# Kernel optimization log

Hardware: AMD Instinct MI355X
Metric: run time of the kernel (lower is better)

## Reference

```python
import jax, jax.numpy as jnp
import numpy as np

N = 50000          # masked node count
E = 800000         # edges (avg degree 16)
IN_DIM, GCN_DIM, REL_DIM, TRAIN_DIM, OUT_DIM = 3, 128, 64, 128, 2
BATCHES = 1


def setup_inputs() -> dict:
    key = jax.random.key(0)
    ks = jax.random.split(key, 16)
    s = 0.05
    return {
        "features": jax.random.normal(ks[0], (N, IN_DIM), jnp.float32),
        "edge_index": jax.random.randint(ks[1], (2, E), 0, N, dtype=jnp.int32),
        "trainOT": jax.random.normal(ks[2], (TRAIN_DIM,), jnp.float32),
        "W1": jax.random.normal(ks[3], (IN_DIM, GCN_DIM), jnp.float32) * s,
        "b1": jnp.zeros((GCN_DIM,), jnp.float32),
        "W2": jax.random.normal(ks[4], (GCN_DIM, GCN_DIM), jnp.float32) * s,
        "b2": jnp.zeros((GCN_DIM,), jnp.float32),
        "Wq": jax.random.normal(ks[5], (GCN_DIM, REL_DIM), jnp.float32) * s,
        "bq": jnp.zeros((REL_DIM,), jnp.float32),
        "Wk": jax.random.normal(ks[6], (TRAIN_DIM, REL_DIM), jnp.float32) * s,
        "bk": jnp.zeros((REL_DIM,), jnp.float32),
        "Wv": jax.random.normal(ks[7], (GCN_DIM, TRAIN_DIM), jnp.float32) * s,
        "bv": jnp.zeros((TRAIN_DIM,), jnp.float32),
        "Ws": jax.random.normal(ks[8], (TRAIN_DIM, OUT_DIM * N), jnp.float32) * s,
        "bs": jnp.zeros((OUT_DIM * N,), jnp.float32),
    }


def _gcn_conv(x, W, b, src, dst, n):
    """PyG GCNConv: h = D^-1/2 (A+I) D^-1/2 (x W) + b (self-loops already in src/dst)."""
    h = x @ W                                                  # [n, d_out]
    ones = jnp.ones(src.shape[0], dtype=x.dtype)
    deg = jax.ops.segment_sum(ones, dst, num_segments=n)      # in-degree incl. self-loop
    dinv = jnp.where(deg > 0, jax.lax.rsqrt(deg), 0.0)
    norm = dinv[src] * dinv[dst]                               # [E+n]
    msg = h[src] * norm[:, None]                               # gather (dominant traffic)
    return jax.ops.segment_sum(msg, dst, num_segments=n) + b   # scatter-add


def reference(features, edge_index, trainOT, W1, b1, W2, b2, Wq, bq, Wk, bk, Wv, bv, Ws, bs):
    n = features.shape[0]
    loop = jnp.arange(n, dtype=edge_index.dtype)
    src = jnp.concatenate([edge_index[0], loop])
    dst = jnp.concatenate([edge_index[1], loop])

    h1 = jax.nn.relu(_gcn_conv(features, W1, b1, src, dst, n))   # gcn1 + relu
    h2 = _gcn_conv(h1, W2, b2, src, dst, n)                      # gcn2

    q = h2 @ Wq + bq                                             # [n, rel]
    v = h2 @ Wv + bv                                             # [n, train]
    k = trainOT @ Wk + bk                                        # [rel]
    scale = jnp.asarray(Wq.shape[1], q.dtype) ** 0.5
    rel = jax.nn.sigmoid((q @ k) / scale)                        # [n]
    summed_idea = (rel[:, None] * v).sum(axis=0)                 # [train]
    new_trainOT = trainOT + summed_idea
    speak = new_trainOT @ Ws + bs                                # [out_dim * num_nodes]
    out = speak.reshape(BATCHES, -1, OUT_DIM)
    return out, new_trainOT
```

## Files before the change

kernel.cpp:

```cpp
#include <hip/hip_runtime.h>
#include <math.h>

#define O_RPD    (0)
#define O_DINV   (512*1024)
#define O_SMALL  (768*1024)
#define O_Y      (1024*1024)
#define O_RELW   (1280*1024)
#define O_REL    (1536*1024)
#define O_GHD    (1792*1024)
#define O_GHS    (2048*1024)
#define O_GOD    (2304*1024)
#define O_GOS    (2560*1024)
#define O_BSD    (2816*1024)
#define O_BSS    (2944*1024)
#define O_PART   (3072*1024)
#define O_XS     (3712*1024)
#define O_G1     (4608*1024)
#define O_SRTD   (5632*1024)
#define O_SRTS   (9216*1024)
#define O_COLD   (12544*1024)

#define NCHUNK 256

static __device__ __forceinline__ int blockExclScan256(int v, volatile int* lds, int t) {
    int lane = t & 63, wid = t >> 6;
    int incl = v;
#pragma unroll
    for (int off = 1; off < 64; off <<= 1) {
        int n = __shfl_up(incl, off);
        if (lane >= off) incl += n;
    }
    if (lane == 63) lds[wid] = incl;
    __syncthreads();
    if (t == 0) {
        int s = 0;
#pragma unroll
        for (int i = 0; i < 4; ++i) { int x = lds[i]; lds[i] = s; s += x; }
    }
    __syncthreads();
    return lds[wid] + incl - v;
}

__global__ void k_hist(const int* __restrict__ eidx, int* __restrict__ ghD,
                       int* __restrict__ ghS,
                       const float* __restrict__ trainOT, const float* __restrict__ Wq,
                       const float* __restrict__ bq, const float* __restrict__ Wk,
                       const float* __restrict__ bk, const float* __restrict__ W2,
                       const float* __restrict__ b2, float* __restrict__ small,
                       int E, int CS, int NB) {
    int b = blockIdx.x, t = threadIdx.x;
    if (b == NCHUNK) {
        if (blockIdx.y) return;
        __shared__ float kv[64];
        __shared__ float wqk[128];
        __shared__ float fred[256];
        if (t < 64) {
            float acc = bk[t];
            for (int j = 0; j < 128; ++j) acc += trainOT[j] * Wk[j * 64 + t];
            kv[t] = acc;
        }
        __syncthreads();
        if (t < 128) {
            float aq = 0.f;
            for (int c2 = 0; c2 < 64; ++c2) aq += Wq[t * 64 + c2] * kv[c2];
            wqk[t] = aq;
        }
        fred[t] = (t < 64) ? bq[t] * kv[t] : 0.f;
        __syncthreads();
        for (int off = 128; off >= 1; off >>= 1) { if (t < off) fred[t] += fred[t + off]; __syncthreads(); }
        float bqs = fred[0];
        __syncthreads();
        if (t < 128) {
            float a2 = 0.f;
            for (int j = 0; j < 128; ++j) a2 += W2[t * 128 + j] * wqk[j];
            small[t] = a2;
        }
        fred[t] = (t < 128) ? b2[t] * wqk[t] : 0.f;
        __syncthreads();
        for (int off = 128; off >= 1; off >>= 1) { if (t < off) fred[t] += fred[t + off]; __syncthreads(); }
        if (t == 0) small[128] = bqs + fred[0];
        return;
    }
    __shared__ int lh[256];
    const int* arr = blockIdx.y ? eidx : (eidx + E);
    int* gh = blockIdx.y ? ghS : ghD;
    lh[t] = 0; __syncthreads();
    int s = b * CS, e = min(E, s + CS);
    for (int i = s + t; i < e; i += 256) atomicAdd(&lh[arr[i] >> 8], 1);
    __syncthreads();
    if (t < NB) gh[t * NCHUNK + b] = lh[t];
}

__global__ void k_goff(const int* __restrict__ ghD, const int* __restrict__ ghS,
                       int* __restrict__ goD, int* __restrict__ goS,
                       int* __restrict__ bsD, int* __restrict__ bsS, int E, int NB) {
    __shared__ int lred[256];
    __shared__ int lds1[4];
    int nb = blockIdx.x, t = threadIdx.x;
    const int* gh = blockIdx.y ? ghS : ghD;
    int* go = blockIdx.y ? goS : goD;
    int* bs = blockIdx.y ? bsS : bsD;
    int rs = 0;
    if (t < nb) {
        const int4* row = reinterpret_cast<const int4*>(gh + t * NCHUNK);
        for (int i = 0; i < NCHUNK / 4; ++i) { int4 p = row[i]; rs += p.x + p.y + p.z + p.w; }
    }
    lred[t] = rs; __syncthreads();
    for (int off = 128; off >= 1; off >>= 1) { if (t < off) lred[t] += lred[t + off]; __syncthreads(); }
    int base = lred[0];
    __syncthreads();
    if (t == 0) { bs[nb] = base; if (nb == NB - 1) bs[NB] = E; }
    int g = gh[nb * NCHUNK + t];
    int gx = blockExclScan256(g, lds1, t);
    go[nb * NCHUNK + t] = base + gx;
}

__global__ void k_scatter(const int* __restrict__ eidx, const int* __restrict__ goD,
                          const int* __restrict__ goS, unsigned int* __restrict__ srtD,
                          unsigned int* __restrict__ srtS, int E, int CS, int NB) {
    __shared__ int lcur[256];
    int b = blockIdx.x, t = threadIdx.x;
    const int* key = blockIdx.y ? eidx : (eidx + E);
    const int* val = blockIdx.y ? (eidx + E) : eidx;
    const int* go  = blockIdx.y ? goS : goD;
    unsigned int* srt = blockIdx.y ? srtS : srtD;
    if (t < NB) lcur[t] = go[t * NCHUNK + b];
    __syncthreads();
    int s = b * CS, e = min(E, s + CS);
    for (int i = s + t; i < e; i += 256) {
        int k = key[i];
        int pos = atomicAdd(&lcur[k >> 8], 1);
        srt[pos] = ((unsigned int)(k & 255) << 16) | (unsigned int)val[i];
    }
}

__global__ void k_build(const unsigned int* __restrict__ srtD, const int* __restrict__ bsD,
                        int* __restrict__ rpD, int* __restrict__ colD,
                        float* __restrict__ dinv, const float* __restrict__ x,
                        float4* __restrict__ xs4, int N) {
    __shared__ int lcnt[256];
    __shared__ int lpos[256];
    __shared__ int lds1[4];
    int nb = blockIdx.x, t = threadIdx.x;
    lcnt[t] = 0; __syncthreads();
    int s = bsD[nb], e = bsD[nb + 1];
    for (int i = s + t; i < e; i += 256) atomicAdd(&lcnt[srtD[i] >> 16], 1);
    __syncthreads();
    int c = lcnt[t];
    int cx = blockExclScan256(c, lds1, t);
    int rpv = s + cx;
    int node = (nb << 8) + t;
    rpD[node] = rpv;
    lpos[t] = rpv;
    if (node < N) {
        float d = rsqrtf((float)(c + 1));
        dinv[node] = d;
        float4 v;
        v.x = x[node * 3] * d; v.y = x[node * 3 + 1] * d; v.z = x[node * 3 + 2] * d; v.w = 0.f;
        xs4[node] = v;
    }
    __syncthreads();
    for (int i = s + t; i < e; i += 256) {
        unsigned int v = srtD[i];
        int p = atomicAdd(&lpos[v >> 16], 1);
        colD[p] = (int)(v & 0xffffu);
    }
}

__global__ void k_y(const float4* __restrict__ xs4, const int* __restrict__ rpD,
                    const int* __restrict__ colD, const float* __restrict__ dinv,
                    const float* __restrict__ W1, const float* __restrict__ b1,
                    const float* __restrict__ small, float4* __restrict__ g1,
                    float* __restrict__ y, int N) {
    int t = threadIdx.x;
    int sub = t & 15;
    int node = blockIdx.x * 16 + (t >> 4);
    if (node >= N) return;
    float di = dinv[node];
    int s = rpD[node], e = rpD[node + 1];
    float a0 = 0.f, a1 = 0.f, a2 = 0.f;
    for (int j = s + sub; j < e; j += 16) {
        float4 xv = xs4[colD[j]];
        a0 += xv.x; a1 += xv.y; a2 += xv.z;
    }
    if (sub == 0) { float4 xv = xs4[node]; a0 += xv.x; a1 += xv.y; a2 += xv.z; }
#pragma unroll
    for (int off = 1; off < 16; off <<= 1) {
        a0 += __shfl_xor(a0, off);
        a1 += __shfl_xor(a1, off);
        a2 += __shfl_xor(a2, off);
    }
    a0 *= di; a1 *= di; a2 *= di;
    float yl = 0.f;
#pragma unroll
    for (int m = 0; m < 8; ++m) {
        int c = sub * 8 + m;
        float h = fmaxf(a0 * W1[c] + a1 * W1[128 + c] + a2 * W1[256 + c] + b1[c], 0.f);
        yl += h * small[c];
    }
#pragma unroll
    for (int off = 1; off < 16; off <<= 1) yl += __shfl_xor(yl, off);
    if (sub == 0) {
        y[node] = yl * di;
        float4 gv; gv.x = a0; gv.y = a1; gv.z = a2; gv.w = di;
        g1[node] = gv;
    }
}

__global__ void k_dv(const float* __restrict__ y, const int* __restrict__ rpD,
                     const int* __restrict__ colD, const float* __restrict__ dinv,
                     const float* __restrict__ small, float* __restrict__ relw,
                     float* __restrict__ rel, int N) {
    int t = threadIdx.x;
    int sub = t & 15;
    int node = blockIdx.x * 16 + (t >> 4);
    if (node >= N) return;
    float di = dinv[node];
    int s = rpD[node], e = rpD[node + 1];
    float acc = (sub == 0) ? y[node] : 0.f;
    for (int j = s + sub; j < e; j += 16) acc += y[colD[j]];
#pragma unroll
    for (int off = 1; off < 16; off <<= 1) acc += __shfl_xor(acc, off);
    float z = (acc * di + small[128]) * 0.125f;
    float r = 1.f / (1.f + __expf(-z));
    if (sub == 0) { rel[node] = r; relw[node] = r * di; }
}

__global__ void k_zS(const unsigned int* __restrict__ srtS, const int* __restrict__ bsS,
                     const float* __restrict__ relw, const float* __restrict__ rel,
                     const float4* __restrict__ g1, const float* __restrict__ W1,
                     const float* __restrict__ b1, float* __restrict__ part, int N) {
    __shared__ float zl[256];
    __shared__ float W1s[384];
    __shared__ float b1s[128];
    __shared__ float sS[4][132];
    int nb = blockIdx.x, t = threadIdx.x, lane = t & 63, wid = t >> 6;
    int sub = lane & 15, gid = wid * 4 + (lane >> 4);
    int node0 = (nb << 8) + t;
    zl[t] = (node0 < N) ? relw[node0] : 0.f;
    if (t < 128) { W1s[t] = W1[t]; W1s[128 + t] = W1[128 + t]; W1s[256 + t] = W1[256 + t];
                   b1s[t] = b1[t]; }
    __syncthreads();
    int s = bsS[nb], e = bsS[nb + 1];
    for (int i = s + t; i < e; i += 256) {
        unsigned int v = srtS[i];
        atomicAdd(&zl[v >> 16], relw[v & 0xffffu]);
    }
    __syncthreads();
    float sacc[8];
#pragma unroll
    for (int m = 0; m < 8; ++m) sacc[m] = 0.f;
    float Racc = 0.f;
#pragma unroll 4
    for (int r = 0; r < 16; ++r) {
        int nl = gid * 16 + r;
        int node = (nb << 8) + nl;
        if (node < N) {
            float4 gv = g1[node];
            float zw = zl[nl] * gv.w;
#pragma unroll
            for (int m = 0; m < 8; ++m) {
                int c = sub * 8 + m;
                float h = fmaxf(gv.x * W1s[c] + gv.y * W1s[128 + c] + gv.z * W1s[256 + c] + b1s[c], 0.f);
                sacc[m] += zw * h;
            }
            if (sub == 0) Racc += rel[node];
        }
    }
#pragma unroll
    for (int m = 0; m < 8; ++m) {
        sacc[m] += __shfl_xor(sacc[m], 16);
        sacc[m] += __shfl_xor(sacc[m], 32);
    }
    Racc += __shfl_xor(Racc, 16);
    Racc += __shfl_xor(Racc, 32);
    if (lane < 16) {
#pragma unroll
        for (int m = 0; m < 8; ++m) sS[wid][sub * 8 + m] = sacc[m];
    }
    if (lane == 0) sS[wid][128] = Racc;
    __syncthreads();
    if (t < 129) part[nb * 132 + t] = sS[0][t] + sS[1][t] + sS[2][t] + sS[3][t];
}

__global__ void k_reduce_part(const float* __restrict__ part, int nblocks, float* __restrict__ small) {
    int c = blockIdx.x;
    float acc = 0.f;
    for (int b = threadIdx.x; b < nblocks; b += blockDim.x) acc += part[b * 132 + c];
    __shared__ float sd[256];
    sd[threadIdx.x] = acc; __syncthreads();
    for (int off = 128; off; off >>= 1) { if (threadIdx.x < off) sd[threadIdx.x] += sd[threadIdx.x + off]; __syncthreads(); }
    if (threadIdx.x == 0) small[132 + c] = sd[0];
}

__global__ void k_tinytail(const float* __restrict__ trainOT, const float* __restrict__ W2,
                           const float* __restrict__ b2, const float* __restrict__ Wv,
                           const float* __restrict__ bv, float* __restrict__ small,
                           float* __restrict__ out_tail) {
    __shared__ float partial[1024];
    __shared__ float Ss[128];
    __shared__ float t1[128];
    int t = threadIdx.x;
    int o = t & 127, sl = t >> 7;
    if (t < 128) Ss[t] = small[132 + t];
    __syncthreads();
    float R = small[260];
    float acc = 0.f;
#pragma unroll
    for (int j = sl * 16; j < sl * 16 + 16; ++j) acc += Ss[j] * W2[j * 128 + o];
    partial[t] = acc; __syncthreads();
    if (t < 128) {
        float v = R * b2[t];
#pragma unroll
        for (int k = 0; k < 8; ++k) v += partial[t + 128 * k];
        t1[t] = v;
    }
    __syncthreads();
    float acc2 = 0.f;
#pragma unroll
    for (int j = sl * 16; j < sl * 16 + 16; ++j) acc2 += t1[j] * Wv[j * 128 + o];
    partial[t] = acc2; __syncthreads();
    if (t < 128) {
        float v = R * bv[t];
#pragma unroll
        for (int k = 0; k < 8; ++k) v += partial[t + 128 * k];
        float nt = trainOT[t] + v;
        small[264 + t] = nt;
        out_tail[t] = nt;
    }
}

__global__ void k_speak(const float* __restrict__ Ws, const float* __restrict__ bs,
                        const float* __restrict__ small, float* __restrict__ out, int out_n) {
    __shared__ float nt[128];
    __shared__ float s0[256], s1[256];
    int t = threadIdx.x;
    if (t < 128) nt[t] = small[264 + t];
    __syncthreads();
    int jj = (t & 63) * 2, sl = t >> 6;
    int j = blockIdx.x * 128 + jj;
    float a0 = 0.f, a1 = 0.f;
    if (j < out_n) {
        const float* w = Ws + (size_t)(sl * 32) * out_n + j;
        for (int k = 0; k < 32; ++k) {
            float cv = nt[sl * 32 + k];
            float2 r = *reinterpret_cast<const float2*>(w + (size_t)k * out_n);
            a0 += cv * r.x; a1 += cv * r.y;
        }
    }
    s0[t] = a0; s1[t] = a1; __syncthreads();
    if (t < 64 && j < out_n) {
        out[j]     = s0[t] + s0[t + 64] + s0[t + 128] + s0[t + 192] + bs[j];
        out[j + 1] = s1[t] + s1[t + 64] + s1[t + 128] + s1[t + 192] + bs[j + 1];
    }
}

extern "C" void kernel_launch(void* const* d_in, const int* in_sizes, int n_in,
                              void* d_out, int out_size, void* d_ws, size_t ws_size,
                              hipStream_t stream) {
    const float* features = (const float*)d_in[0];
    const int*   eidx     = (const int*)d_in[1];
    const float* trainOT  = (const float*)d_in[2];
    const float* W1 = (const float*)d_in[3];
    const float* b1 = (const float*)d_in[4];
    const float* W2 = (const float*)d_in[5];
    const float* b2 = (const float*)d_in[6];
    const float* Wq = (const float*)d_in[7];
    const float* bq = (const float*)d_in[8];
    const float* Wk = (const float*)d_in[9];
    const float* bk = (const float*)d_in[10];
    const float* Wv = (const float*)d_in[11];
    const float* bv = (const float*)d_in[12];
    const float* Ws = (const float*)d_in[13];
    const float* bs = (const float*)d_in[14];

    int N = in_sizes[0] / 3;
    int E = in_sizes[1] / 2;
    int NB = (N + 255) >> 8;
    int CS = (E + NCHUNK - 1) / NCHUNK;

    char* ws = (char*)d_ws;
    int*   rpD   = (int*)(ws + O_RPD);
    float* dinv  = (float*)(ws + O_DINV);
    float* small = (float*)(ws + O_SMALL);
    float* y     = (float*)(ws + O_Y);
    float* relw  = (float*)(ws + O_RELW);
    float* rel   = (float*)(ws + O_REL);
    int*   ghD   = (int*)(ws + O_GHD);
    int*   ghS   = (int*)(ws + O_GHS);
    int*   goD   = (int*)(ws + O_GOD);
    int*   goS   = (int*)(ws + O_GOS);
    int*   bsD   = (int*)(ws + O_BSD);
    int*   bsS   = (int*)(ws + O_BSS);
    float* part  = (float*)(ws + O_PART);
    float4* xs4  = (float4*)(ws + O_XS);
    float4* g1   = (float4*)(ws + O_G1);
    unsigned int* srtD = (unsigned int*)(ws + O_SRTD);
    unsigned int* srtS = (unsigned int*)(ws + O_SRTS);
    int*   colD  = (int*)(ws + O_COLD);
    float* out   = (float*)d_out;
    int out_n = out_size - 128;

    k_hist<<<dim3(NCHUNK + 1, 2), 256, 0, stream>>>(eidx, ghD, ghS,
                                                    trainOT, Wq, bq, Wk, bk, W2, b2, small,
                                                    E, CS, NB);
    k_goff<<<dim3(NB, 2), 256, 0, stream>>>(ghD, ghS, goD, goS, bsD, bsS, E, NB);
    k_scatter<<<dim3(NCHUNK, 2), 256, 0, stream>>>(eidx, goD, goS, srtD, srtS, E, CS, NB);
    k_build<<<NB, 256, 0, stream>>>(srtD, bsD, rpD, colD, dinv, features, xs4, N);
    k_y<<<(N + 15) / 16, 256, 0, stream>>>(xs4, rpD, colD, dinv, W1, b1, small, g1, y, N);
    k_dv<<<(N + 15) / 16, 256, 0, stream>>>(y, rpD, colD, dinv, small, relw, rel, N);
    k_zS<<<NB, 256, 0, stream>>>(srtS, bsS, relw, rel, g1, W1, b1, part, N);
    k_reduce_part<<<129, 256, 0, stream>>>(part, NB, small);
    k_tinytail<<<1, 1024, 0, stream>>>(trainOT, W2, b2, Wv, bv, small, out + out_n);
    k_speak<<<(out_n + 127) / 128, 256, 0, stream>>>(Ws, bs, small, out, out_n);
}
```

Before: 98.84 us.

## Merge dst/src histogram and scatter passes, fold partial reduction into tail kernel

The histogram and scatter kernels now handle both the destination-keyed and source-keyed bucketing in one pass over the edge list instead of two y-blocks. Each edge is read once and feeds both LDS counters. The k_reduce_part launch is removed: k_zS writes partials transposed and k_tinytail reduces them directly with a single 1024-thread block. This saves one launch and some edge re-reads, at the cost of halving grid parallelism in hist/scatter and running the final reduction on a single block.

```diff
diff --git a/kernel.cpp b/kernel.cpp
--- a/kernel.cpp
+++ b/kernel.cpp
@@ -50,7 +50,6 @@
                        int E, int CS, int NB) {
     int b = blockIdx.x, t = threadIdx.x;
     if (b == NCHUNK) {
-        if (blockIdx.y) return;
         __shared__ float kv[64];
         __shared__ float wqk[128];
         __shared__ float fred[256];
@@ -81,14 +80,21 @@
         if (t == 0) small[128] = bqs + fred[0];
         return;
     }
-    __shared__ int lh[256];
-    const int* arr = blockIdx.y ? eidx : (eidx + E);
-    int* gh = blockIdx.y ? ghS : ghD;
-    lh[t] = 0; __syncthreads();
+    __shared__ int lhD[256];
+    __shared__ int lhS[256];
+    const int* src = eidx;
+    const int* dst = eidx + E;
+    lhD[t] = 0; lhS[t] = 0; __syncthreads();
     int s = b * CS, e = min(E, s + CS);
-    for (int i = s + t; i < e; i += 256) atomicAdd(&lh[arr[i] >> 8], 1);
-    __syncthreads();
-    if (t < NB) gh[t * NCHUNK + b] = lh[t];
+    for (int i = s + t; i < e; i += 256) {
+        atomicAdd(&lhD[dst[i] >> 8], 1);
+        atomicAdd(&lhS[src[i] >> 8], 1);
+    }
+    __syncthreads();
+    if (t < NB) {
+        ghD[t * NCHUNK + b] = lhD[t];
+        ghS[t * NCHUNK + b] = lhS[t];
+    }
 }
 
 __global__ void k_goff(const int* __restrict__ ghD, const int* __restrict__ ghS,
@@ -118,19 +124,23 @@
 __global__ void k_scatter(const int* __restrict__ eidx, const int* __restrict__ goD,
                           const int* __restrict__ goS, unsigned int* __restrict__ srtD,
                           unsigned int* __restrict__ srtS, int E, int CS, int NB) {
-    __shared__ int lcur[256];
+    __shared__ int lcurD[256];
+    __shared__ int lcurS[256];
     int b = blockIdx.x, t = threadIdx.x;
-    const int* key = blockIdx.y ? eidx : (eidx + E);
-    const int* val = blockIdx.y ? (eidx + E) : eidx;
-    const int* go  = blockIdx.y ? goS : goD;
-    unsigned int* srt = blockIdx.y ? srtS : srtD;
-    if (t < NB) lcur[t] = go[t * NCHUNK + b];
+    const int* src = eidx;
+    const int* dst = eidx + E;
+    if (t < NB) {
+        lcurD[t] = goD[t * NCHUNK + b];
+        lcurS[t] = goS[t * NCHUNK + b];
+    }
     __syncthreads();
     int s = b * CS, e = min(E, s + CS);
     for (int i = s + t; i < e; i += 256) {
-        int k = key[i];
-        int pos = atomicAdd(&lcur[k >> 8], 1);
-        srt[pos] = ((unsigned int)(k & 255) << 16) | (unsigned int)val[i];
+        int sv = src[i], dv = dst[i];
+        int pD = atomicAdd(&lcurD[dv >> 8], 1);
+        srtD[pD] = ((unsigned int)(dv & 255) << 16) | (unsigned int)sv;
+        int pS = atomicAdd(&lcurS[sv >> 8], 1);
+        srtS[pS] = ((unsigned int)(sv & 255) << 16) | (unsigned int)dv;
     }
 }
 
@@ -280,35 +290,45 @@
     }
     if (lane == 0) sS[wid][128] = Racc;
     __syncthreads();
-    if (t < 129) part[nb * 132 + t] = sS[0][t] + sS[1][t] + sS[2][t] + sS[3][t];
-}
-
-__global__ void k_reduce_part(const float* __restrict__ part, int nblocks, float* __restrict__ small) {
-    int c = blockIdx.x;
-    float acc = 0.f;
-    for (int b = threadIdx.x; b < nblocks; b += blockDim.x) acc += part[b * 132 + c];
-    __shared__ float sd[256];
-    sd[threadIdx.x] = acc; __syncthreads();
-    for (int off = 128; off; off >>= 1) { if (threadIdx.x < off) sd[threadIdx.x] += sd[threadIdx.x + off]; __syncthreads(); }
-    if (threadIdx.x == 0) small[132 + c] = sd[0];
+    if (t < 129) part[t * 256 + nb] = sS[0][t] + sS[1][t] + sS[2][t] + sS[3][t];
 }
 
 __global__ void k_tinytail(const float* __restrict__ trainOT, const float* __restrict__ W2,
                            const float* __restrict__ b2, const float* __restrict__ Wv,
-                           const float* __restrict__ bv, float* __restrict__ small,
-                           float* __restrict__ out_tail) {
+                           const float* __restrict__ bv, const float* __restrict__ part,
+                           float* __restrict__ small, float* __restrict__ out_tail, int NB) {
     __shared__ float partial[1024];
     __shared__ float Ss[128];
     __shared__ float t1[128];
+    __shared__ float r8[8];
     int t = threadIdx.x;
-    int o = t & 127, sl = t >> 7;
-    if (t < 128) Ss[t] = small[132 + t];
-    __syncthreads();
-    float R = small[260];
-    float acc = 0.f;
-#pragma unroll
-    for (int j = sl * 16; j < sl * 16 + 16; ++j) acc += Ss[j] * W2[j * 128 + o];
-    partial[t] = acc; __syncthreads();
+    {
+        int c = t >> 3, sl = t & 7;
+        float s = 0.f;
+        for (int nb = sl; nb < NB; nb += 8) s += part[c * 256 + nb];
+        partial[t] = s;
+        if (t < 8) {
+            float r = 0.f;
+            for (int nb = t; nb < NB; nb += 8) r += part[128 * 256 + nb];
+            r8[t] = r;
+        }
+    }
+    __syncthreads();
+    if (t < 128) {
+        float v = 0.f;
+#pragma unroll
+        for (int k = 0; k < 8; ++k) v += partial[t * 8 + k];
+        Ss[t] = v;
+    }
+    __shared__ float Rsh;
+    if (t == 0) Rsh = r8[0] + r8[1] + r8[2] + r8[3] + r8[4] + r8[5] + r8[6] + r8[7];
+    __syncthreads();
+    float R = Rsh;
+    int o = t & 127, sl2 = t >> 7;
+    float a1 = 0.f;
+#pragma unroll
+    for (int j = sl2 * 16; j < sl2 * 16 + 16; ++j) a1 += Ss[j] * W2[j * 128 + o];
+    partial[t] = a1; __syncthreads();
     if (t < 128) {
         float v = R * b2[t];
 #pragma unroll
@@ -316,10 +336,10 @@
         t1[t] = v;
     }
     __syncthreads();
-    float acc2 = 0.f;
-#pragma unroll
-    for (int j = sl * 16; j < sl * 16 + 16; ++j) acc2 += t1[j] * Wv[j * 128 + o];
-    partial[t] = acc2; __syncthreads();
+    float a2 = 0.f;
+#pragma unroll
+    for (int j = sl2 * 16; j < sl2 * 16 + 16; ++j) a2 += t1[j] * Wv[j * 128 + o];
+    partial[t] = a2; __syncthreads();
     if (t < 128) {
         float v = R * bv[t];
 #pragma unroll
@@ -401,16 +421,14 @@
     float* out   = (float*)d_out;
     int out_n = out_size - 128;
 
-    k_hist<<<dim3(NCHUNK + 1, 2), 256, 0, stream>>>(eidx, ghD, ghS,
-                                                    trainOT, Wq, bq, Wk, bk, W2, b2, small,
-                                                    E, CS, NB);
+    k_hist<<<NCHUNK + 1, 256, 0, stream>>>(eidx, ghD, ghS,
+                                           trainOT, Wq, bq, Wk, bk, W2, b2, small, E, CS, NB);
     k_goff<<<dim3(NB, 2), 256, 0, stream>>>(ghD, ghS, goD, goS, bsD, bsS, E, NB);
-    k_scatter<<<dim3(NCHUNK, 2), 256, 0, stream>>>(eidx, goD, goS, srtD, srtS, E, CS, NB);
+    k_scatter<<<NCHUNK, 256, 0, stream>>>(eidx, goD, goS, srtD, srtS, E, CS, NB);
     k_build<<<NB, 256, 0, stream>>>(srtD, bsD, rpD, colD, dinv, features, xs4, N);
     k_y<<<(N + 15) / 16, 256, 0, stream>>>(xs4, rpD, colD, dinv, W1, b1, small, g1, y, N);
     k_dv<<<(N + 15) / 16, 256, 0, stream>>>(y, rpD, colD, dinv, small, relw, rel, N);
     k_zS<<<NB, 256, 0, stream>>>(srtS, bsS, relw, rel, g1, W1, b1, part, N);
-    k_reduce_part<<<129, 256, 0, stream>>>(part, NB, small);
-    k_tinytail<<<1, 1024, 0, stream>>>(trainOT, W2, b2, Wv, bv, small, out + out_n);
+    k_tinytail<<<1, 1024, 0, stream>>>(trainOT, W2, b2, Wv, bv, part, small, out + out_n, NB);
     k_speak<<<(out_n + 127) / 128, 256, 0, stream>>>(Ws, bs, small, out, out_n);
 }
```

Measured after the change: 103.6 us. 1.05x slower.

## Fuse partial reduction and tiny tail into speak kernel, redundantly per block

Applied to the files above, without the earlier changes.

Removes the k_reduce_part and k_tinytail launches. Every k_speak block now reduces the per-block partials and runs the two 128x128 matvecs itself. The partials layout is transposed to column-major with a stride of 256 so each row can be summed with float4 loads. This saves two launches and their serialization gaps, but every one of the ~782 blocks repeats the reduction and matvecs (W2 and Wv reads mostly hit cache). It also assumes NB<=256.

```diff
diff --git a/kernel.cpp b/kernel.cpp
--- a/kernel.cpp
+++ b/kernel.cpp
@@ -280,62 +280,42 @@
     }
     if (lane == 0) sS[wid][128] = Racc;
     __syncthreads();
-    if (t < 129) part[nb * 132 + t] = sS[0][t] + sS[1][t] + sS[2][t] + sS[3][t];
-}
-
-__global__ void k_reduce_part(const float* __restrict__ part, int nblocks, float* __restrict__ small) {
-    int c = blockIdx.x;
-    float acc = 0.f;
-    for (int b = threadIdx.x; b < nblocks; b += blockDim.x) acc += part[b * 132 + c];
-    __shared__ float sd[256];
-    sd[threadIdx.x] = acc; __syncthreads();
-    for (int off = 128; off; off >>= 1) { if (threadIdx.x < off) sd[threadIdx.x] += sd[threadIdx.x + off]; __syncthreads(); }
-    if (threadIdx.x == 0) small[132 + c] = sd[0];
-}
-
-__global__ void k_tinytail(const float* __restrict__ trainOT, const float* __restrict__ W2,
-                           const float* __restrict__ b2, const float* __restrict__ Wv,
-                           const float* __restrict__ bv, float* __restrict__ small,
-                           float* __restrict__ out_tail) {
-    __shared__ float partial[1024];
-    __shared__ float Ss[128];
+    if (t < 129) part[t * 256 + nb] = sS[0][t] + sS[1][t] + sS[2][t] + sS[3][t];
+}
+
+__global__ void k_speak(const float* __restrict__ Ws, const float* __restrict__ bs,
+                        const float* __restrict__ trainOT, const float* __restrict__ W2,
+                        const float* __restrict__ b2, const float* __restrict__ Wv,
+                        const float* __restrict__ bv, const float* __restrict__ part,
+                        float* __restrict__ out, int out_n, int NB) {
+    __shared__ float Ss[129];
     __shared__ float t1[128];
-    int t = threadIdx.x;
-    int o = t & 127, sl = t >> 7;
-    if (t < 128) Ss[t] = small[132 + t];
-    __syncthreads();
-    float R = small[260];
-    float acc = 0.f;
-#pragma unroll
-    for (int j = sl * 16; j < sl * 16 + 16; ++j) acc += Ss[j] * W2[j * 128 + o];
-    partial[t] = acc; __syncthreads();
-    if (t < 128) {
-        float v = R * b2[t];
-#pragma unroll
-        for (int k = 0; k < 8; ++k) v += partial[t + 128 * k];
-        t1[t] = v;
-    }
-    __syncthreads();
-    float acc2 = 0.f;
-#pragma unroll
-    for (int j = sl * 16; j < sl * 16 + 16; ++j) acc2 += t1[j] * Wv[j * 128 + o];
-    partial[t] = acc2; __syncthreads();
-    if (t < 128) {
-        float v = R * bv[t];
-#pragma unroll
-        for (int k = 0; k < 8; ++k) v += partial[t + 128 * k];
-        float nt = trainOT[t] + v;
-        small[264 + t] = nt;
-        out_tail[t] = nt;
-    }
-}
-
-__global__ void k_speak(const float* __restrict__ Ws, const float* __restrict__ bs,
-                        const float* __restrict__ small, float* __restrict__ out, int out_n) {
     __shared__ float nt[128];
     __shared__ float s0[256], s1[256];
     int t = threadIdx.x;
-    if (t < 128) nt[t] = small[264 + t];
+    if (t < 129) {
+        const float4* p4 = reinterpret_cast<const float4*>(part + t * 256);
+        float a = 0.f;
+        int n4 = NB >> 2;
+        for (int i = 0; i < n4; ++i) { float4 v = p4[i]; a += v.x + v.y + v.z + v.w; }
+        for (int i = n4 << 2; i < NB; ++i) a += part[t * 256 + i];
+        Ss[t] = a;
+    }
+    __syncthreads();
+    float R = Ss[128];
+    if (t < 128) {
+        float a = R * b2[t];
+        for (int j = 0; j < 128; ++j) a += Ss[j] * W2[j * 128 + t];
+        t1[t] = a;
+    }
+    __syncthreads();
+    if (t < 128) {
+        float a = R * bv[t];
+        for (int j = 0; j < 128; ++j) a += t1[j] * Wv[j * 128 + t];
+        float v = trainOT[t] + a;
+        nt[t] = v;
+        if (blockIdx.x == 0) out[out_n + t] = v;
+    }
     __syncthreads();
     int jj = (t & 63) * 2, sl = t >> 6;
     int j = blockIdx.x * 128 + jj;
@@ -410,7 +390,6 @@
     k_y<<<(N + 15) / 16, 256, 0, stream>>>(xs4, rpD, colD, dinv, W1, b1, small, g1, y, N);
     k_dv<<<(N + 15) / 16, 256, 0, stream>>>(y, rpD, colD, dinv, small, relw, rel, N);
     k_zS<<<NB, 256, 0, stream>>>(srtS, bsS, relw, rel, g1, W1, b1, part, N);
-    k_reduce_part<<<129, 256, 0, stream>>>(part, NB, small);
-    k_tinytail<<<1, 1024, 0, stream>>>(trainOT, W2, b2, Wv, bv, small, out + out_n);
-    k_speak<<<(out_n + 127) / 128, 256, 0, stream>>>(Ws, bs, small, out, out_n);
-}
+    k_speak<<<(out_n + 127) / 128, 256, 0, stream>>>(Ws, bs, trainOT, W2, b2, Wv, bv,
+                                                     part, out, out_n, NB);
+}
```

Measured after the change: 109.2 us. 10.5% more time.
